# Performance work log

Measured on AMD Instinct MI355X. Metric: run time of the kernel, lower is better.

The kernel has to match this reference:

```python
import jax, jax.numpy as jnp
import numpy as np

IN_FEATURES = 1024
OUT_FEATURES = 1024


def setup_inputs() -> dict:
    key = jax.random.key(0)
    k1, k2, k3, k4 = jax.random.split(key, 4)
    input = jax.random.normal(k1, (4096, IN_FEATURES), dtype=jnp.float32)
    mask = jax.random.uniform(k2, (512, 512, 512), dtype=jnp.float32)
    # nn.Linear params: weight [out, in], bias [out]
    bound = 1.0 / np.sqrt(IN_FEATURES)
    weight = jax.random.uniform(k3, (OUT_FEATURES, IN_FEATURES), dtype=jnp.float32,
                                minval=-bound, maxval=bound)
    bias = jax.random.uniform(k4, (OUT_FEATURES,), dtype=jnp.float32,
                              minval=-bound, maxval=bound)
    return {"input": input, "mask": mask, "weight": weight, "bias": bias}


def reference(input, mask, weight, bias):
    # LINEAR PASS: out = input @ W^T + b  -> [batch, out_features]
    out = jnp.einsum('bi,oi->bo', input, weight) + bias
    # scalar threshold = mean over batch of per-row sums
    threshold = out.sum(axis=1).mean()
    # The torch module extracts indices via host-side np.argwhere (data-dependent
    # shape). The jit-compatible device-side equivalent is the boolean mask of
    # elements exceeding the threshold; indices are recoverable via nonzero.
    hi_mask = mask > threshold
    return (out, hi_mask)
```

## Files before the change

kernel.cpp:

```cpp
#include <hip/hip_runtime.h>
#include <hip/hip_bf16.h>

#define M_ROWS 4096
#define N_OUT  1024
#define K_IN   1024
#define MASK_N 134217728

__device__ inline short f2bf(float f) {
    unsigned u = __float_as_uint(f);
    unsigned r = u + 0x7fffu + ((u >> 16) & 1u);
    return (short)(r >> 16);
}

__device__ inline float next_up(float f) {
    unsigned u = __float_as_uint(f);
    if (u == 0x80000000u || u == 0u) return __uint_as_float(0x00000001u);
    if (f > 0.0f) return __uint_as_float(u + 1u);
    return __uint_as_float(u - 1u);
}

__global__ __launch_bounds__(256) void colsum_kernel(
    const float* __restrict__ input, const float* __restrict__ weight,
    double* __restrict__ s_in, double* __restrict__ w_sum)
{
    int b = blockIdx.x;
    int t = threadIdx.x;
    const float* src;
    double* dst;
    int row0;
    if (b < 32) { src = input;  dst = s_in;  row0 = b * 128; }
    else        { src = weight; dst = w_sum; row0 = (b - 32) * 128; }
    for (int c = 0; c < 4; ++c) {
        int col = t + c * 256;
        double acc = 0.0;
        for (int r = 0; r < 128; ++r)
            acc += (double)src[(size_t)(row0 + r) * 1024 + col];
        atomicAdd(&dst[col], acc);
    }
}

__global__ __launch_bounds__(1024) void threshold_kernel(
    const double* __restrict__ s_in, const double* __restrict__ w_sum,
    const float* __restrict__ bias, double* __restrict__ thr, float* __restrict__ cut)
{
    __shared__ double red[1024];
    int t = threadIdx.x;
    double v = s_in[t] * w_sum[t] * (1.0 / 4096.0) + (double)bias[t];
    red[t] = v;
    __syncthreads();
    for (int s = 512; s > 0; s >>= 1) {
        if (t < s) red[t] += red[t + s];
        __syncthreads();
    }
    if (t == 0) {
        double th = red[0];
        *thr = th;
        float f = (float)th;
        if ((double)f <= th) f = next_up(f);
        *cut = f;
    }
}

typedef __attribute__((ext_vector_type(8))) short bf16x8;
typedef __attribute__((ext_vector_type(4))) float f32x4;

#define LDA 40

__global__ __launch_bounds__(256) void gemm_kernel(
    const float* __restrict__ A,
    const float* __restrict__ W,
    const float* __restrict__ bias,
    float* __restrict__ C)
{
    __shared__ short As[128 * LDA];
    __shared__ short Bs[128 * LDA];

    const int tid  = threadIdx.x;
    const int wave = tid >> 6;
    const int lane = tid & 63;
    const int quad = lane >> 4;
    const int l16  = lane & 15;
    const int wr   = (wave >> 1) * 64;
    const int wc   = (wave & 1) * 64;

    const int tile_m = (blockIdx.x >> 3) * 128;
    const int tile_n = (blockIdx.x & 7) * 128;

    f32x4 acc[4][4];
    for (int i = 0; i < 4; ++i)
        for (int j = 0; j < 4; ++j)
            acc[i][j] = (f32x4){0.f, 0.f, 0.f, 0.f};

    for (int k0 = 0; k0 < K_IN; k0 += 32) {
        for (int it = 0; it < 4; ++it) {
            int f   = tid + it * 256;
            int row = f >> 3;
            int c4  = (f & 7) << 2;
            float4 av = *(const float4*)&A[(size_t)(tile_m + row) * K_IN + k0 + c4];
            float4 bv = *(const float4*)&W[(size_t)(tile_n + row) * K_IN + k0 + c4];
            short4 a4 = { f2bf(av.x), f2bf(av.y), f2bf(av.z), f2bf(av.w) };
            short4 b4 = { f2bf(bv.x), f2bf(bv.y), f2bf(bv.z), f2bf(bv.w) };
            *(short4*)&As[row * LDA + c4] = a4;
            *(short4*)&Bs[row * LDA + c4] = b4;
        }
        __syncthreads();

        bf16x8 af[4], bfr[4];
        for (int i = 0; i < 4; ++i) {
            af[i]  = *(const bf16x8*)&As[(wr + i * 16 + l16) * LDA + quad * 8];
            bfr[i] = *(const bf16x8*)&Bs[(wc + i * 16 + l16) * LDA + quad * 8];
        }
        for (int i = 0; i < 4; ++i)
            for (int j = 0; j < 4; ++j)
                acc[i][j] = __builtin_amdgcn_mfma_f32_16x16x32_bf16(
                    af[i], bfr[j], acc[i][j], 0, 0, 0);
        __syncthreads();
    }

    for (int i = 0; i < 4; ++i) {
        for (int j = 0; j < 4; ++j) {
            int col = tile_n + wc + j * 16 + l16;
            float b = bias[col];
            for (int r = 0; r < 4; ++r) {
                int row = tile_m + wr + i * 16 + quad * 4 + r;
                C[(size_t)row * N_OUT + col] = acc[i][j][r] + b;
            }
        }
    }
}

__global__ __launch_bounds__(256) void mask_kernel(
    const float4* __restrict__ mask, float4* __restrict__ out,
    const float* __restrict__ cut_p, int n4)
{
    float cut = *cut_p;
    int i = blockIdx.x * blockDim.x + threadIdx.x;
    int stride = gridDim.x * blockDim.x;
    for (; i < n4; i += stride) {
        float4 m = mask[i];
        float4 o;
        o.x = (m.x >= cut) ? 1.0f : 0.0f;
        o.y = (m.y >= cut) ? 1.0f : 0.0f;
        o.z = (m.z >= cut) ? 1.0f : 0.0f;
        o.w = (m.w >= cut) ? 1.0f : 0.0f;
        out[i] = o;
    }
}

extern "C" void kernel_launch(void* const* d_in, const int* in_sizes, int n_in,
                              void* d_out, int out_size, void* d_ws, size_t ws_size,
                              hipStream_t stream) {
    const float* input  = (const float*)d_in[0];
    const float* mask   = (const float*)d_in[1];
    const float* weight = (const float*)d_in[2];
    const float* bias   = (const float*)d_in[3];

    float* out = (float*)d_out;
    float* hi  = out + (size_t)M_ROWS * N_OUT;

    double* s_in  = (double*)d_ws;
    double* w_sum = s_in + 1024;
    double* thr   = w_sum + 1024;
    float*  cut   = (float*)(thr + 1);

    hipMemsetAsync(d_ws, 0, 2048 * sizeof(double), stream);

    colsum_kernel<<<40, 256, 0, stream>>>(input, weight, s_in, w_sum);
    threshold_kernel<<<1, 1024, 0, stream>>>(s_in, w_sum, bias, thr, cut);
    gemm_kernel<<<256, 256, 0, stream>>>(input, weight, bias, out);
    mask_kernel<<<16384, 256, 0, stream>>>((const float4*)mask, (float4*)hi,
                                           cut, MASK_N / 4);
}
```

Before: 946.6 us.

## Pre-convert operands to bf16 with swizzle, async LDS loads in GEMM, nontemporal mask

Merges the fp32-to-bf16 conversion into the column-sum pass, writing swizzled bf16 copies of input and weight to workspace. The GEMM then fills LDS through global_load_lds direct async copies with an XOR swizzle, so it no longer reloads and reconverts fp32 tiles on every k-step. The mask kernel switches to nontemporal loads and stores so the large streaming traffic bypasses the cache. The cost is an extra bf16 write and read pass, and the column-sum launch grows to many more blocks issuing atomics.

New measurement: 904.3 us. 4.5% less time.

```diff
diff --git a/kernel.cpp b/kernel.cpp
--- a/kernel.cpp
+++ b/kernel.cpp
@@ -1,10 +1,15 @@
 #include <hip/hip_runtime.h>
 #include <hip/hip_bf16.h>
+#include <stdint.h>
 
 #define M_ROWS 4096
 #define N_OUT  1024
 #define K_IN   1024
 #define MASK_N 134217728
+
+typedef __attribute__((ext_vector_type(8))) short bf16x8;
+typedef __attribute__((ext_vector_type(4))) float f32x4;
+typedef float f4v __attribute__((ext_vector_type(4)));
 
 __device__ inline short f2bf(float f) {
     unsigned u = __float_as_uint(f);
@@ -19,24 +24,41 @@
     return __uint_as_float(u - 1u);
 }
 
-__global__ __launch_bounds__(256) void colsum_kernel(
+__device__ inline void async16(const void* g, void* l) {
+    __builtin_amdgcn_global_load_lds(
+        (const __attribute__((address_space(1))) unsigned int*)g,
+        (__attribute__((address_space(3))) unsigned int*)l, 16, 0, 0);
+}
+
+__global__ __launch_bounds__(256) void conv_colsum_kernel(
     const float* __restrict__ input, const float* __restrict__ weight,
+    short* __restrict__ in_bf, short* __restrict__ w_bf,
     double* __restrict__ s_in, double* __restrict__ w_sum)
 {
     int b = blockIdx.x;
     int t = threadIdx.x;
-    const float* src;
-    double* dst;
-    int row0;
-    if (b < 32) { src = input;  dst = s_in;  row0 = b * 128; }
-    else        { src = weight; dst = w_sum; row0 = (b - 32) * 128; }
-    for (int c = 0; c < 4; ++c) {
-        int col = t + c * 256;
-        double acc = 0.0;
-        for (int r = 0; r < 128; ++r)
-            acc += (double)src[(size_t)(row0 + r) * 1024 + col];
-        atomicAdd(&dst[col], acc);
+    const float* src; short* dst; double* sums; int row0;
+    if (b < 256) { src = input;  dst = in_bf; sums = s_in;  row0 = b * 16; }
+    else         { src = weight; dst = w_bf;  sums = w_sum; row0 = (b - 256) * 16; }
+
+    const int kc = t >> 3;
+    const int c  = (t >> 1) & 3;
+    const int j0 = (t & 1) << 2;
+
+    double a0 = 0, a1 = 0, a2 = 0, a3 = 0;
+    for (int r = 0; r < 16; ++r) {
+        int R = row0 + r;
+        float4 v = *(const float4*)&src[(size_t)R * 1024 + 4 * t];
+        int sc = c ^ ((R >> 1) & 3);
+        short4 s4 = { f2bf(v.x), f2bf(v.y), f2bf(v.z), f2bf(v.w) };
+        *(short4*)&dst[(size_t)R * 1024 + (kc << 5) + (sc << 3) + j0] = s4;
+        a0 += (double)v.x; a1 += (double)v.y; a2 += (double)v.z; a3 += (double)v.w;
     }
+    int c0 = 4 * t;
+    atomicAdd(&sums[c0 + 0], a0);
+    atomicAdd(&sums[c0 + 1], a1);
+    atomicAdd(&sums[c0 + 2], a2);
+    atomicAdd(&sums[c0 + 3], a3);
 }
 
 __global__ __launch_bounds__(1024) void threshold_kernel(
@@ -61,19 +83,14 @@
     }
 }
 
-typedef __attribute__((ext_vector_type(8))) short bf16x8;
-typedef __attribute__((ext_vector_type(4))) float f32x4;
-
-#define LDA 40
-
 __global__ __launch_bounds__(256) void gemm_kernel(
-    const float* __restrict__ A,
-    const float* __restrict__ W,
+    const short* __restrict__ Abf,
+    const short* __restrict__ Wbf,
     const float* __restrict__ bias,
     float* __restrict__ C)
 {
-    __shared__ short As[128 * LDA];
-    __shared__ short Bs[128 * LDA];
+    __shared__ short As[128 * 32];
+    __shared__ short Bs[128 * 32];
 
     const int tid  = threadIdx.x;
     const int wave = tid >> 6;
@@ -91,24 +108,24 @@
         for (int j = 0; j < 4; ++j)
             acc[i][j] = (f32x4){0.f, 0.f, 0.f, 0.f};
 
+    const short* gA = Abf + (size_t)(tile_m + (tid >> 2)) * 1024 + ((tid & 3) << 3);
+    const short* gB = Wbf + (size_t)(tile_n + (tid >> 2)) * 1024 + ((tid & 3) << 3);
+    short* lA = &As[tid * 8];
+    short* lB = &Bs[tid * 8];
+
     for (int k0 = 0; k0 < K_IN; k0 += 32) {
-        for (int it = 0; it < 4; ++it) {
-            int f   = tid + it * 256;
-            int row = f >> 3;
-            int c4  = (f & 7) << 2;
-            float4 av = *(const float4*)&A[(size_t)(tile_m + row) * K_IN + k0 + c4];
-            float4 bv = *(const float4*)&W[(size_t)(tile_n + row) * K_IN + k0 + c4];
-            short4 a4 = { f2bf(av.x), f2bf(av.y), f2bf(av.z), f2bf(av.w) };
-            short4 b4 = { f2bf(bv.x), f2bf(bv.y), f2bf(bv.z), f2bf(bv.w) };
-            *(short4*)&As[row * LDA + c4] = a4;
-            *(short4*)&Bs[row * LDA + c4] = b4;
-        }
+        async16(gA + k0,             lA);
+        async16(gA + 64 * 1024 + k0, lA + 64 * 32);
+        async16(gB + k0,             lB);
+        async16(gB + 64 * 1024 + k0, lB + 64 * 32);
         __syncthreads();
 
         bf16x8 af[4], bfr[4];
         for (int i = 0; i < 4; ++i) {
-            af[i]  = *(const bf16x8*)&As[(wr + i * 16 + l16) * LDA + quad * 8];
-            bfr[i] = *(const bf16x8*)&Bs[(wc + i * 16 + l16) * LDA + quad * 8];
+            int ra = wr + i * 16 + l16;
+            af[i]  = *(const bf16x8*)&As[ra * 32 + ((quad ^ ((ra >> 1) & 3)) << 3)];
+            int rb = wc + i * 16 + l16;
+            bfr[i] = *(const bf16x8*)&Bs[rb * 32 + ((quad ^ ((rb >> 1) & 3)) << 3)];
         }
         for (int i = 0; i < 4; ++i)
             for (int j = 0; j < 4; ++j)
@@ -130,20 +147,20 @@
 }
 
 __global__ __launch_bounds__(256) void mask_kernel(
-    const float4* __restrict__ mask, float4* __restrict__ out,
+    const f4v* __restrict__ mask, f4v* __restrict__ out,
     const float* __restrict__ cut_p, int n4)
 {
     float cut = *cut_p;
     int i = blockIdx.x * blockDim.x + threadIdx.x;
     int stride = gridDim.x * blockDim.x;
     for (; i < n4; i += stride) {
-        float4 m = mask[i];
-        float4 o;
+        f4v m = __builtin_nontemporal_load(&mask[i]);
+        f4v o;
         o.x = (m.x >= cut) ? 1.0f : 0.0f;
         o.y = (m.y >= cut) ? 1.0f : 0.0f;
         o.z = (m.z >= cut) ? 1.0f : 0.0f;
         o.w = (m.w >= cut) ? 1.0f : 0.0f;
-        out[i] = o;
+        __builtin_nontemporal_store(o, &out[i]);
     }
 }
 
@@ -158,16 +175,18 @@
     float* out = (float*)d_out;
     float* hi  = out + (size_t)M_ROWS * N_OUT;
 
-    double* s_in  = (double*)d_ws;
-    double* w_sum = s_in + 1024;
-    double* thr   = w_sum + 1024;
-    float*  cut   = (float*)(thr + 1);
+    char* wsb = (char*)d_ws;
+    double* s_in  = (double*)wsb;
+    double* w_sum = (double*)(wsb + 8192);
+    double* thr   = (double*)(wsb + 16384);
+    float*  cut   = (float*)(wsb + 16384 + 8);
+    short*  in_bf = (short*)(wsb + 32768);
+    short*  w_bf  = (short*)(wsb + 32768 + (size_t)M_ROWS * K_IN * 2);
 
-    hipMemsetAsync(d_ws, 0, 2048 * sizeof(double), stream);
+    hipMemsetAsync(d_ws, 0, 16384, stream);
 
-    colsum_kernel<<<40, 256, 0, stream>>>(input, weight, s_in, w_sum);
+    conv_colsum_kernel<<<320, 256, 0, stream>>>(input, weight, in_bf, w_bf, s_in, w_sum);
     threshold_kernel<<<1, 1024, 0, stream>>>(s_in, w_sum, bias, thr, cut);
-    gemm_kernel<<<256, 256, 0, stream>>>(input, weight, bias, out);
-    mask_kernel<<<16384, 256, 0, stream>>>((const float4*)mask, (float4*)hi,
-                                           cut, MASK_N / 4);
+    gemm_kernel<<<256, 256, 0, stream>>>(in_bf, w_bf, bias, out);
+    mask_kernel<<<16384, 256, 0, stream>>>((const f4v*)mask, (f4v*)hi, cut, MASK_N / 4);
 }
```
